# Performance work log

Measured on AMD Instinct MI355X. Metric: run time of the kernel, lower is better.

## Reference

```python
import jax, jax.numpy as jnp
import numpy as np

N, DIM, HEADS, E = 20000, 256, 4, 100000
C = DIM  # TransformerConv out_channels per head (concat=False averages heads)


def setup_inputs() -> dict:
    key = jax.random.key(0)
    ks = jax.random.split(key, 12)
    s = DIM ** -0.5
    w = lambda k, shape: jax.random.normal(k, shape, jnp.float32) * s
    z = lambda shape: jnp.zeros(shape, jnp.float32)
    return {
        "f_all": jax.random.normal(ks[0], (N, DIM), jnp.float32),
        "edge_index": jax.random.randint(ks[1], (2, E), 0, N),
        "W_gcn": w(ks[2], (DIM, DIM)), "b_gcn": z((DIM,)),
        "W_q": w(ks[3], (DIM, HEADS * C)), "b_q": z((HEADS * C,)),
        "W_k": w(ks[4], (DIM, HEADS * C)), "b_k": z((HEADS * C,)),
        "W_v": w(ks[5], (DIM, HEADS * C)), "b_v": z((HEADS * C,)),
        "W_skip": w(ks[6], (DIM, DIM)), "b_skip": z((DIM,)),
        "W_beta": w(ks[7], (3 * DIM, 1)),
        "W_cnn": w(ks[8], (DIM, DIM)), "b_cnn": z((DIM,)),
    }


def reference(f_all, edge_index, W_gcn, b_gcn, W_q, b_q, W_k, b_k, W_v, b_v,
              W_skip, b_skip, W_beta, W_cnn, b_cnn):
    src, dst = edge_index[0], edge_index[1]

    # --- GCNConv: add self loops, symmetric D^-1/2 (A+I) D^-1/2 normalization ---
    loop = jnp.arange(N)
    s2 = jnp.concatenate([src, loop])
    d2 = jnp.concatenate([dst, loop])
    deg = jax.ops.segment_sum(jnp.ones_like(d2, jnp.float32), d2, N)
    dinv = jnp.where(deg > 0, 1.0 / jnp.sqrt(deg), 0.0)
    norm = dinv[s2] * dinv[d2]                    # [E+N]
    h = f_all @ W_gcn                             # [N, DIM]
    x = jax.ops.segment_sum(h[s2] * norm[:, None], d2, N) + b_gcn
    x = jax.nn.relu(x)

    # --- TransformerConv(heads=H, concat=False, beta=True) ---
    q = (x @ W_q + b_q).reshape(N, HEADS, C)
    k = (x @ W_k + b_k).reshape(N, HEADS, C)
    v = (x @ W_v + b_v).reshape(N, HEADS, C)
    logits = jnp.einsum('ehc,ehc->eh', q[dst], k[src]) / np.float32(np.sqrt(C))
    m = jax.ops.segment_max(logits, dst, N)       # per-target max for stable softmax
    e = jnp.exp(logits - m[dst])
    denom = jax.ops.segment_sum(e, dst, N)
    alpha = e / jnp.maximum(denom[dst], 1e-16)    # [E, H]
    agg = jax.ops.segment_sum(v[src] * alpha[:, :, None], dst, N)  # [N, H, C]
    out = agg.mean(axis=1)                        # concat=False -> head average
    xr = x @ W_skip + b_skip                      # root/skip branch
    beta = jax.nn.sigmoid(jnp.concatenate([out, xr, out - xr], axis=-1) @ W_beta)
    tf = jax.nn.relu(beta * xr + (1.0 - beta) * out)  # [N, DIM]

    # --- Conv1d with kernel (dim,1) on [1,1,dim,N]: per-node linear, output [dim,N] ---
    conv = jnp.einsum('cd,nd->cn', W_cnn, tf) + b_cnn[:, None]  # [DIM, N]
    # torch does .view(1, n_mole, -1) on the [1,dim,1,N] conv output: raw reshape
    return conv.reshape(1, N, DIM)
```

## Files before the change

### kernel.cpp

```cpp
#include <hip/hip_runtime.h>
#include <math.h>

#define DIMC 256
#define NHEAD 4
#define CAP 64

typedef unsigned short bf16u;
typedef __attribute__((ext_vector_type(8))) short bf16x8;
typedef __attribute__((ext_vector_type(4))) float f32x4;

typedef __attribute__((address_space(1))) const unsigned char ga_u8;
typedef __attribute__((address_space(3))) unsigned char lds_u8;
__device__ __forceinline__ void gld_lds16(const void* g, void* l) {
    __builtin_amdgcn_global_load_lds((ga_u8*)g, (lds_u8*)l, 16, 0, 0);
}

__device__ __forceinline__ float bf2f(bf16u u) {
    union { float f; unsigned int i; } c; c.i = ((unsigned int)u) << 16; return c.f;
}
__device__ __forceinline__ bf16u f2bf(float f) {
    union { float f; unsigned int i; } c; c.f = f;
    unsigned int r = c.i + 0x7fffu + ((c.i >> 16) & 1u);
    return (bf16u)(r >> 16);
}
__device__ __forceinline__ void store_bf4(bf16u* p, float4 v) {
    ushort4 raw;
    raw.x = f2bf(v.x); raw.y = f2bf(v.y); raw.z = f2bf(v.z); raw.w = f2bf(v.w);
    *(ushort4*)p = raw;
}
__device__ __forceinline__ void load_bf8(const bf16u* p, float* o) {
    bf16x8 raw = *(const bf16x8*)p;
#pragma unroll
    for (int i = 0; i < 8; ++i) {
        union { float f; unsigned int u; } c;
        c.u = ((unsigned int)(unsigned short)raw[i]) << 16;
        o[i] = c.f;
    }
}
__device__ __forceinline__ void store_bf8(bf16u* p, const float* v) {
    bf16x8 raw;
#pragma unroll
    for (int i = 0; i < 8; ++i) raw[i] = (short)f2bf(v[i]);
    *(bf16x8*)p = raw;
}


__global__ void fill_kernel(const int* __restrict__ src, const int* __restrict__ dst,
                            int* __restrict__ cursor, int* __restrict__ srcs, int E) {
    int e = blockIdx.x * 256 + threadIdx.x;
    if (e < E) {
        int d = dst[e];
        int pos = atomicAdd(&cursor[d], 1);
        if (pos < CAP) srcs[d * CAP + pos] = src[e];
    }
}


__global__ __launch_bounds__(256) void prep_kernel(
    const float* __restrict__ f_all, int n4_f,
    const float* __restrict__ W_gcn, const float* __restrict__ W_q,
    const float* __restrict__ W_k, const float* __restrict__ W_v,
    const float* __restrict__ W_skip, const float* __restrict__ W_cnn,
    const float* __restrict__ b_q, const float* __restrict__ b_v,
    const float* __restrict__ b_skip,
    bf16u* __restrict__ xbuf, bf16u* __restrict__ WgcnT,
    bf16u* __restrict__ BTyp, bf16u* __restrict__ BT_vs,
    bf16u* __restrict__ Wcnn_b,
    float* __restrict__ ybias, float* __restrict__ bvm,
    int* __restrict__ cursor, int N) {
    __shared__ __align__(16) char sh[40960];
    int b = blockIdx.x, t = threadIdx.x;
    int nf = (n4_f + 255) >> 8;
    int nz = (N + 255) >> 8;

    if (b < 16) {
        bf16u (*As)[128][32] = (bf16u(*)[128][32])sh;
        bf16u (*Bs)[128][32] = (bf16u(*)[128][32])(sh + 16384);
        bf16u (*Cs)[128]     = (bf16u(*)[128])(sh + 32768);
        int rb = b >> 1, cb = b & 1;
        int h = rb >> 1;
        int j0 = (rb & 1) * 128;
        int t0 = h * 256;
        int w = t >> 6, lane = t & 63;
        int q = lane >> 4, r = lane & 15;
        int wm = (w & 1) * 64, wn = (w >> 1) * 64;
        int srow = t >> 2, scol = (t & 3) * 8;
        const float* ak0 = W_k + (size_t)(j0 + srow) * 1024 + t0 + scol;
        const float* ak1 = W_k + (size_t)(j0 + 64 + srow) * 1024 + t0 + scol;
        const float* bq0 = W_q + (size_t)(cb * 128 + srow) * 1024 + t0 + scol;
        const float* bq1 = W_q + (size_t)(cb * 128 + 64 + srow) * 1024 + t0 + scol;
        auto stage = [&](const float* gp, bf16u* lp) {
            float4 u = *(const float4*)gp, v = *(const float4*)(gp + 4);
            bf16x8 o;
            o[0] = (short)f2bf(u.x); o[1] = (short)f2bf(u.y);
            o[2] = (short)f2bf(u.z); o[3] = (short)f2bf(u.w);
            o[4] = (short)f2bf(v.x); o[5] = (short)f2bf(v.y);
            o[6] = (short)f2bf(v.z); o[7] = (short)f2bf(v.w);
            *(bf16x8*)lp = o;
        };
        f32x4 acc[4][4] = {};
        for (int g = 0; g < 4; ++g) {
            int k0 = g * 64;
            stage(ak0 + k0,      &As[0][srow][scol]);
            stage(ak1 + k0,      &As[0][64 + srow][scol]);
            stage(ak0 + k0 + 32, &As[1][srow][scol]);
            stage(ak1 + k0 + 32, &As[1][64 + srow][scol]);
            stage(bq0 + k0,      &Bs[0][srow][scol]);
            stage(bq1 + k0,      &Bs[0][64 + srow][scol]);
            stage(bq0 + k0 + 32, &Bs[1][srow][scol]);
            stage(bq1 + k0 + 32, &Bs[1][64 + srow][scol]);
            __syncthreads();
#pragma unroll
            for (int ks = 0; ks < 2; ++ks) {
                bf16x8 af[4], bfr[4];
#pragma unroll
                for (int i = 0; i < 4; ++i) af[i] = *(const bf16x8*)&As[ks][wm + i * 16 + r][q * 8];
#pragma unroll
                for (int j = 0; j < 4; ++j) bfr[j] = *(const bf16x8*)&Bs[ks][wn + j * 16 + r][q * 8];
#pragma unroll
                for (int i = 0; i < 4; ++i)
#pragma unroll
                    for (int j = 0; j < 4; ++j)
                        acc[i][j] = __builtin_amdgcn_mfma_f32_16x16x32_bf16(af[i], bfr[j], acc[i][j], 0, 0, 0);
            }
            __syncthreads();
        }
        int bm = rb * 128, bn = cb * 128;
        int rhalf = (w & 1) * 16;
        int colbase = (w >> 1) * 64;
#pragma unroll
        for (int i = 0; i < 4; ++i) {
#pragma unroll
            for (int j = 0; j < 4; ++j)
#pragma unroll
                for (int rg = 0; rg < 4; ++rg)
                    Cs[rhalf + q * 4 + rg][colbase + j * 16 + r] = f2bf(acc[i][j][rg] * 0.0625f);
            __syncthreads();
#pragma unroll
            for (int cpass = 0; cpass < 2; ++cpass) {
                int chunk = cpass * 256 + t;
                int sr = chunk >> 4;
                int c16 = chunk & 15;
                int grow = bm + (sr < 16 ? i * 16 + sr : 64 + i * 16 + (sr - 16));
                *(bf16x8*)&BTyp[(size_t)grow * 256 + bn + c16 * 8] = *(const bf16x8*)&Cs[sr][c16 * 8];
            }
            __syncthreads();
        }
        return;
    }
    b -= 16;
    if (b < nf) {
        int i = b * 256 + t;
        if (i < n4_f) {
            float4 vv = *(const float4*)(f_all + (size_t)i * 4);
            store_bf4(xbuf + (size_t)i * 4, vv);
        }
        return;
    }
    b -= nf;
    if (b < 64) {
        int i = b * 256 + t;
        float4 vv = *(const float4*)(W_cnn + (size_t)i * 4);
        store_bf4(Wcnn_b + (size_t)i * 4, vv);
        return;
    }
    b -= 64;
    if (b < 4) {
        int h = b, j = t;
        const float4* bq4 = (const float4*)(b_q + h * 256);
        const float4* wk4 = (const float4*)(W_k + (size_t)j * 1024 + h * 256);
        float acc = 0.f;
        for (int u = 0; u < 64; ++u) {
            float4 a = bq4[u], w = wk4[u];
            acc += a.x * w.x + a.y * w.y + a.z * w.z + a.w * w.w;
        }
        ybias[h * 256 + j] = acc * 0.0625f;
        return;
    }
    b -= 4;
    if (b < 1) {
        ybias[1024 + t] = b_skip[t];
        bvm[t] = 0.25f * (b_v[t] + b_v[256 + t] + b_v[512 + t] + b_v[768 + t]);
        return;
    }
    b -= 1;
    if (b < nz) {
        int i = b * 256 + t;
        if (i < N) cursor[i] = 0;
        return;
    }
    b -= nz;
    float (*T)[33] = (float(*)[33])sh;
    const float* src; bf16u* dst;
    int inld, inrow0, incol0, outld, outrow0, outcol0;
    if (b < 64) {
        int N0 = (b & 7) * 32, K0 = (b >> 3) * 32;
        src = W_gcn; inld = 256; inrow0 = K0; incol0 = N0;
        dst = WgcnT; outld = 256; outrow0 = N0; outcol0 = K0;
    } else if (b < 128) {
        int bb = b - 64; int N0 = (bb & 7) * 32, K0 = (bb >> 3) * 32;
        src = W_skip; inld = 256; inrow0 = K0; incol0 = N0;
        dst = BTyp;  outld = 256; outrow0 = 1024 + N0; outcol0 = K0;
    } else {
        int bb = b - 128; int jt = bb & 7, ct = (bb >> 3) & 7, hh = bb >> 6;
        src = W_v;  inld = 1024; inrow0 = ct * 32; incol0 = hh * 256 + jt * 32;
        dst = BT_vs; outld = 1024; outrow0 = jt * 32; outcol0 = hh * 256 + ct * 32;
    }
    int tx = t & 31, ty = t >> 5;
#pragma unroll
    for (int i = 0; i < 4; ++i)
        T[ty + 8 * i][tx] = src[(size_t)(inrow0 + ty + 8 * i) * inld + incol0 + tx];
    __syncthreads();
#pragma unroll
    for (int i = 0; i < 4; ++i)
        dst[(size_t)(outrow0 + ty + 8 * i) * outld + outcol0 + tx] = f2bf(T[tx][ty + 8 * i]);
}


template <bool ROWBIAS>
__global__ __launch_bounds__(256) void gemm_tile(const bf16u* __restrict__ A,
                                                 const bf16u* __restrict__ BT,
                                                 const float* __restrict__ bias,
                                                 void* __restrict__ Cout,
                                                 int M, int Nc, int ldc, int K) {
    __shared__ __align__(16) bf16u As[2][128][32];
    __shared__ __align__(16) bf16u Bs[2][128][32];
    int t = threadIdx.x;
    int w = t >> 6, lane = t & 63;
    int q = lane >> 4, r = lane & 15;
    int wm = (w & 1) * 64, wn = (w >> 1) * 64;
    int bm = blockIdx.y * 128, bn = blockIdx.x * 128;

    int srow = t >> 2, scol = (t & 3) * 8;
    int arow0 = bm + srow;      if (arow0 >= M)  arow0 = M - 1;
    int arow1 = bm + 64 + srow; if (arow1 >= M)  arow1 = M - 1;
    int brow0 = bn + srow;      if (brow0 >= Nc) brow0 = Nc - 1;
    int brow1 = bn + 64 + srow; if (brow1 >= Nc) brow1 = Nc - 1;
    const bf16u* a0 = A + (size_t)arow0 * K + scol;
    const bf16u* a1 = A + (size_t)arow1 * K + scol;
    const bf16u* b0 = BT + (size_t)brow0 * K + scol;
    const bf16u* b1 = BT + (size_t)brow1 * K + scol;

    char* As_base = (char*)&As[0][0][0] + w * 1024;
    char* Bs_base = (char*)&Bs[0][0][0] + w * 1024;

    f32x4 acc[4][4] = {};
    int ngroups = K >> 6;
    for (int g = 0; g < ngroups; ++g) {
        int k0 = g * 64;
        gld_lds16(a0 + k0, As_base);
        gld_lds16(a1 + k0, As_base + 4096);
        gld_lds16(b0 + k0, Bs_base);
        gld_lds16(b1 + k0, Bs_base + 4096);
        gld_lds16(a0 + k0 + 32, As_base + 8192);
        gld_lds16(a1 + k0 + 32, As_base + 8192 + 4096);
        gld_lds16(b0 + k0 + 32, Bs_base + 8192);
        gld_lds16(b1 + k0 + 32, Bs_base + 8192 + 4096);
        __syncthreads();
#pragma unroll
        for (int ks = 0; ks < 2; ++ks) {
            bf16x8 af[4], bfr[4];
#pragma unroll
            for (int i = 0; i < 4; ++i) af[i] = *(const bf16x8*)&As[ks][wm + i * 16 + r][q * 8];
#pragma unroll
            for (int j = 0; j < 4; ++j) bfr[j] = *(const bf16x8*)&Bs[ks][wn + j * 16 + r][q * 8];
#pragma unroll
            for (int i = 0; i < 4; ++i)
#pragma unroll
                for (int j = 0; j < 4; ++j)
                    acc[i][j] = __builtin_amdgcn_mfma_f32_16x16x32_bf16(af[i], bfr[j], acc[i][j], 0, 0, 0);
        }
        __syncthreads();
    }

    if (ROWBIAS) {
        float* C = (float*)Cout;
#pragma unroll
        for (int j = 0; j < 4; ++j) {
            int col = bn + wn + j * 16 + r;
            if (col >= Nc) continue;
#pragma unroll
            for (int i = 0; i < 4; ++i)
#pragma unroll
                for (int rg = 0; rg < 4; ++rg) {
                    int row = bm + wm + i * 16 + q * 4 + rg;
                    if (row < M)
                        __builtin_nontemporal_store(acc[i][j][rg] + bias[row],
                                                    &C[(size_t)row * ldc + col]);
                }
        }
    } else {
        __shared__ __align__(16) bf16u Cs[32][128];
        bf16u* C = (bf16u*)Cout;
        float cb4[4];
#pragma unroll
        for (int j = 0; j < 4; ++j) {
            int col = bn + wn + j * 16 + r;
            cb4[j] = bias ? bias[col] : 0.0f;
        }
        int rhalf = (w & 1) * 16;
        int colbase = (w >> 1) * 64;
        __syncthreads();
#pragma unroll
        for (int i = 0; i < 4; ++i) {
#pragma unroll
            for (int j = 0; j < 4; ++j)
#pragma unroll
                for (int rg = 0; rg < 4; ++rg)
                    Cs[rhalf + q * 4 + rg][colbase + j * 16 + r] = f2bf(acc[i][j][rg] + cb4[j]);
            __syncthreads();
#pragma unroll
            for (int cpass = 0; cpass < 2; ++cpass) {
                int chunk = cpass * 256 + t;
                int sr = chunk >> 4;
                int c16 = chunk & 15;
                int grow = bm + (sr < 16 ? i * 16 + sr : 64 + i * 16 + (sr - 16));
                if (grow < M)
                    __builtin_nontemporal_store(*(const bf16x8*)&Cs[sr][c16 * 8],
                                                (bf16x8*)&C[(size_t)grow * ldc + bn + c16 * 8]);
            }
            __syncthreads();
        }
    }
}


__global__ __launch_bounds__(256, 1) void zout_kernel(const bf16u* __restrict__ Z,
                                                      const bf16u* __restrict__ BT_vs,
                                                      const bf16u* __restrict__ Yp, int ldy,
                                                      const float* __restrict__ bvm,
                                                      const float* __restrict__ W_beta,
                                                      const int* __restrict__ cursor,
                                                      bf16u* __restrict__ tf, int M) {
    __shared__ __align__(16) char sh[53248];
    bf16u (*As)[128][32] = (bf16u(*)[128][32])sh;
    bf16u (*Bs)[256][32] = (bf16u(*)[256][32])(sh + 16384);
    bf16u (*Xr)[256]     = (bf16u(*)[256])sh;
    bf16u (*Cs)[256]     = (bf16u(*)[256])(sh + 16384);
    float* gateL = (float*)(sh + 49152);
    float* w13L  = (float*)(sh + 49664);
    float* w23L  = (float*)(sh + 50688);
    float* bvmL  = (float*)(sh + 51712);
    float* redL  = (float*)(sh + 52736);
    float* betL  = (float*)(sh + 52992);

    int t = threadIdx.x;
    int w = t >> 6, lane = t & 63;
    int q = lane >> 4, r = lane & 15;
    int wm = (w & 1) * 64, wmIdx = w & 1;
    int cg = w >> 1;
    int bm = blockIdx.x * 128;

    {
        float w1 = W_beta[t], w2 = W_beta[256 + t], w3 = W_beta[512 + t];
        w13L[t] = w1 + w3;
        w23L[t] = w2 - w3;
        bvmL[t] = bvm[t];
        if (t < 128) {
            int row = bm + t; if (row >= M) row = M - 1;
            gateL[t] = (cursor[row] > 0) ? 1.f : 0.f;
        }
    }

    int srow = t >> 2, scol = (t & 3) * 8;
    int arow0 = bm + srow;      if (arow0 >= M) arow0 = M - 1;
    int arow1 = bm + 64 + srow; if (arow1 >= M) arow1 = M - 1;
    const bf16u* a0 = Z + (size_t)arow0 * 1024 + scol;
    const bf16u* a1 = Z + (size_t)arow1 * 1024 + scol;
    const bf16u* bp[4];
#pragma unroll
    for (int h = 0; h < 4; ++h) bp[h] = BT_vs + (size_t)(h * 64 + srow) * 1024 + scol;

    char* As_base = (char*)sh + w * 1024;
    char* Bs_base = (char*)sh + 16384 + w * 1024;

    f32x4 acc[4][8] = {};
    for (int g = 0; g < 16; ++g) {
        int k0 = g * 64;
        gld_lds16(a0 + k0, As_base);
        gld_lds16(a1 + k0, As_base + 4096);
        gld_lds16(a0 + k0 + 32, As_base + 8192);
        gld_lds16(a1 + k0 + 32, As_base + 8192 + 4096);
#pragma unroll
        for (int h = 0; h < 4; ++h) {
            gld_lds16(bp[h] + k0, Bs_base + h * 4096);
            gld_lds16(bp[h] + k0 + 32, Bs_base + 16384 + h * 4096);
        }
        __syncthreads();
#pragma unroll
        for (int ks = 0; ks < 2; ++ks) {
            bf16x8 af[4], bfr[8];
#pragma unroll
            for (int i = 0; i < 4; ++i) af[i] = *(const bf16x8*)&As[ks][wm + i * 16 + r][q * 8];
#pragma unroll
            for (int j = 0; j < 8; ++j) {
                int brow = (j < 4 ? cg * 64 + j * 16 : 128 + cg * 64 + (j - 4) * 16) + r;
                bfr[j] = *(const bf16x8*)&Bs[ks][brow][q * 8];
            }
#pragma unroll
            for (int i = 0; i < 4; ++i)
#pragma unroll
                for (int j = 0; j < 8; ++j)
                    acc[i][j] = __builtin_amdgcn_mfma_f32_16x16x32_bf16(af[i], bfr[j], acc[i][j], 0, 0, 0);
        }
        __syncthreads();
    }

#pragma unroll
    for (int i = 0; i < 4; ++i) {
#pragma unroll
        for (int p = 0; p < 4; ++p) {
            int idx = p * 256 + t;
            int rowl = idx >> 5, ch = idx & 31;
            int grow = bm + (rowl < 16 ? i * 16 + rowl : 64 + i * 16 + (rowl - 16));
            if (grow >= M) grow = M - 1;
            gld_lds16(Yp + (size_t)grow * ldy + 1024 + ch * 8,
                      (char*)sh + p * 4096 + w * 1024);
        }
        __syncthreads();

        float contrib[4] = {0.f, 0.f, 0.f, 0.f};
#pragma unroll
        for (int j = 0; j < 8; ++j) {
            int col = (j < 4 ? cg * 64 + j * 16 : 128 + cg * 64 + (j - 4) * 16) + r;
            float w13c = w13L[col], w23c = w23L[col], bvc = bvmL[col];
#pragma unroll
            for (int rg = 0; rg < 4; ++rg) {
                int rowl32 = wmIdx * 16 + q * 4 + rg;
                float ov = acc[i][j][rg] + gateL[wm + i * 16 + q * 4 + rg] * bvc;
                float xr = bf2f(Xr[rowl32][col]);
                contrib[rg] += ov * w13c + xr * w23c;
            }
        }
#pragma unroll
        for (int rg = 0; rg < 4; ++rg)
#pragma unroll
            for (int msk = 1; msk <= 8; msk <<= 1)
                contrib[rg] += __shfl_xor(contrib[rg], msk, 64);
        if (r == 0) {
#pragma unroll
            for (int rg = 0; rg < 4; ++rg)
                redL[cg * 32 + wmIdx * 16 + q * 4 + rg] = contrib[rg];
        }
        __syncthreads();
        if (t < 32) betL[t] = 1.f / (1.f + __expf(-(redL[t] + redL[32 + t])));
        __syncthreads();

#pragma unroll
        for (int j = 0; j < 8; ++j) {
            int col = (j < 4 ? cg * 64 + j * 16 : 128 + cg * 64 + (j - 4) * 16) + r;
            float bvc = bvmL[col];
#pragma unroll
            for (int rg = 0; rg < 4; ++rg) {
                int rowl32 = wmIdx * 16 + q * 4 + rg;
                float bet = betL[rowl32];
                float ov = acc[i][j][rg] + gateL[wm + i * 16 + q * 4 + rg] * bvc;
                float xr = bf2f(Xr[rowl32][col]);
                Cs[rowl32][col] = f2bf(fmaxf(bet * xr + (1.f - bet) * ov, 0.f));
            }
        }
        __syncthreads();
#pragma unroll
        for (int p = 0; p < 4; ++p) {
            int idx = p * 256 + t;
            int sr = idx >> 5, c32 = idx & 31;
            int grow = bm + (sr < 16 ? i * 16 + sr : 64 + i * 16 + (sr - 16));
            if (grow < M)
                __builtin_nontemporal_store(*(const bf16x8*)&Cs[sr][c32 * 8],
                                            (bf16x8*)&tf[(size_t)grow * 256 + c32 * 8]);
        }
        __syncthreads();
    }
}


__global__ __launch_bounds__(256) void gcn_agg_kernel(const bf16u* __restrict__ h,
                                                      const int* __restrict__ cursor,
                                                      const int* __restrict__ srcs,
                                                      const float* __restrict__ b_gcn,
                                                      bf16u* __restrict__ x, int N) {
    int n = blockIdx.x * 8 + (threadIdx.x >> 5);
    if (n >= N) return;
    int lane = threadIdx.x & 31;
    int cb = lane * 8;
    int cnt = cursor[n]; if (cnt > CAP) cnt = CAP;
    float dn = rsqrtf((float)(cnt + 1));
    float hn[8];
    load_bf8(h + (size_t)n * DIMC + cb, hn);
    int base = n * CAP;
    float acc[8] = {};
    int i = 0;
    for (; i + 4 <= cnt; i += 4) {
        int4 s4 = *(const int4*)(srcs + base + i);
        float d0 = rsqrtf((float)(cursor[s4.x] + 1));
        float d1 = rsqrtf((float)(cursor[s4.y] + 1));
        float d2 = rsqrtf((float)(cursor[s4.z] + 1));
        float d3 = rsqrtf((float)(cursor[s4.w] + 1));
        float h0[8], h1[8], h2[8], h3[8];
        load_bf8(h + (size_t)s4.x * DIMC + cb, h0);
        load_bf8(h + (size_t)s4.y * DIMC + cb, h1);
        load_bf8(h + (size_t)s4.z * DIMC + cb, h2);
        load_bf8(h + (size_t)s4.w * DIMC + cb, h3);
#pragma unroll
        for (int j = 0; j < 8; ++j)
            acc[j] += h0[j] * d0 + h1[j] * d1 + h2[j] * d2 + h3[j] * d3;
    }
    for (; i < cnt; ++i) {
        int s = srcs[base + i];
        float ds = rsqrtf((float)(cursor[s] + 1));
        float hv[8];
        load_bf8(h + (size_t)s * DIMC + cb, hv);
#pragma unroll
        for (int j = 0; j < 8; ++j) acc[j] += hv[j] * ds;
    }
    float4 bg0 = *(const float4*)(b_gcn + cb);
    float4 bg1 = *(const float4*)(b_gcn + cb + 4);
    float bg[8] = {bg0.x, bg0.y, bg0.z, bg0.w, bg1.x, bg1.y, bg1.z, bg1.w};
    float dnn = dn * dn;
    float o[8];
#pragma unroll
    for (int j = 0; j < 8; ++j) o[j] = fmaxf(dn * acc[j] + hn[j] * dnn + bg[j], 0.f);
    store_bf8(x + (size_t)n * DIMC + cb, o);
}


__global__ __launch_bounds__(256) void attn_kernel(const bf16u* __restrict__ Y, int ldy,
                                                   const bf16u* __restrict__ x,
                                                   const int* __restrict__ cursor,
                                                   const int* __restrict__ srcs,
                                                   bf16u* __restrict__ Z, int N) {
    __shared__ __align__(16) bf16u xs[4][2][256];
    int wv = threadIdx.x >> 6;
    int n = blockIdx.x * 4 + wv;
    if (n >= N) return;
    int lane = threadIdx.x & 63;
    int hq = lane >> 4;
    int r = lane & 15;

    float yv[16];
    const bf16u* yrow = Y + (size_t)n * ldy + hq * DIMC + r * 16;
    load_bf8(yrow, yv);
    load_bf8(yrow + 8, yv + 8);

    int cnt = cursor[n]; if (cnt > CAP) cnt = CAP;
    int base = n * CAP;
    float m = -INFINITY, denom = 0.f;
    float acc[16];
#pragma unroll
    for (int j = 0; j < 16; ++j) acc[j] = 0.f;

    int rl = lane >> 5;
    int rc = (lane & 31) * 8;
    bf16u* myslot = &xs[wv][rl][rc];

    int iters = (cnt + 1) >> 1;
    int i0 = 0, i1 = 0;
    if (cnt > 1) {
        int2 ss = *(const int2*)(srcs + base);
        i0 = ss.x; i1 = ss.y;
    } else if (cnt == 1) {
        i0 = srcs[base]; i1 = i0;
    }
    bf16x8 raw;
    if (iters > 0)
        raw = *(const bf16x8*)(x + (size_t)(rl ? i1 : i0) * DIMC + rc);

    for (int it = 0; it < iters; ++it) {
        *(bf16x8*)myslot = raw;
        int e2 = (it + 1) * 2;
        int nv2 = cnt - e2;
        if (nv2 > 1) {
            int2 ss = *(const int2*)(srcs + base + e2);
            i0 = ss.x; i1 = ss.y;
        } else if (nv2 == 1) {
            i0 = srcs[base + e2]; i1 = i0;
        }
        if (nv2 > 0)
            raw = *(const bf16x8*)(x + (size_t)(rl ? i1 : i0) * DIMC + rc);
        asm volatile("s_waitcnt lgkmcnt(0)" ::: "memory");
        float x0[16], x1[16];
        load_bf8(&xs[wv][0][r * 16], x0);
        load_bf8(&xs[wv][0][r * 16 + 8], x0 + 8);
        load_bf8(&xs[wv][1][r * 16], x1);
        load_bf8(&xs[wv][1][r * 16 + 8], x1 + 8);
        float d0 = 0.f, d1 = 0.f;
#pragma unroll
        for (int j = 0; j < 16; ++j) { d0 += yv[j] * x0[j]; d1 += yv[j] * x1[j]; }
#pragma unroll
        for (int msk = 1; msk <= 8; msk <<= 1) {
            d0 += __shfl_xor(d0, msk, 64);
            d1 += __shfl_xor(d1, msk, 64);
        }
        if ((cnt & 1) && it == iters - 1) d1 = -INFINITY;
        float pm = fmaxf(d0, d1);
        if (pm > m + 8.f) {
            float so = __expf(m - pm);
            denom *= so;
#pragma unroll
            for (int j = 0; j < 16; ++j) acc[j] *= so;
            m = pm;
        }
        float p0 = __expf(d0 - m);
        float p1 = __expf(d1 - m);
        denom += p0 + p1;
#pragma unroll
        for (int j = 0; j < 16; ++j) acc[j] += p0 * x0[j] + p1 * x1[j];
        asm volatile("" ::: "memory");
    }

    float inv = 0.25f / fmaxf(denom, 1e-16f);
    float o[16];
#pragma unroll
    for (int j = 0; j < 16; ++j) o[j] = acc[j] * inv;
    bf16u* zrow = Z + (size_t)n * 1024 + hq * DIMC + r * 16;
    store_bf8(zrow, o);
    store_bf8(zrow + 8, o + 8);
}


static inline size_t align_up(size_t x) { return (x + 255) & ~(size_t)255; }

extern "C" void kernel_launch(void* const* d_in, const int* in_sizes, int n_in,
                              void* d_out, int out_size, void* d_ws, size_t ws_size,
                              hipStream_t stream) {
    const float* f_all  = (const float*)d_in[0];
    const int*   eidx   = (const int*)d_in[1];
    const float* W_gcn  = (const float*)d_in[2];
    const float* b_gcn  = (const float*)d_in[3];
    const float* W_q    = (const float*)d_in[4];
    const float* b_q    = (const float*)d_in[5];
    const float* W_k    = (const float*)d_in[6];
    const float* W_v    = (const float*)d_in[8];
    const float* b_v    = (const float*)d_in[9];
    const float* W_skip = (const float*)d_in[10];
    const float* b_skip = (const float*)d_in[11];
    const float* W_beta = (const float*)d_in[12];
    const float* W_cnn  = (const float*)d_in[13];
    const float* b_cnn  = (const float*)d_in[14];

    const int N = in_sizes[0] / DIMC;
    const int E = in_sizes[1] / 2;
    const int* src = eidx;
    const int* dst = eidx + E;

    char* p = (char*)d_ws;
    auto alloc = [&](size_t bytes) { char* r = p; p += align_up(bytes); return r; };
    int*   cursor = (int*)alloc((size_t)N * 4);
    int*   srcs   = (int*)alloc((size_t)N * CAP * 4);
    bf16u* WgcnT  = (bf16u*)alloc(256 * 256 * 2);
    bf16u* BTyp   = (bf16u*)alloc((size_t)1280 * 256 * 2);
    bf16u* BT_vs  = (bf16u*)alloc((size_t)256 * 1024 * 2);
    bf16u* Wcnn_b = (bf16u*)alloc(256 * 256 * 2);
    float* ybias  = (float*)alloc(1280 * 4);
    float* bvm    = (float*)alloc(256 * 4);
    bf16u* xbuf   = (bf16u*)alloc((size_t)N * DIMC * 2);
    bf16u* h      = (bf16u*)alloc((size_t)N * DIMC * 2);
    bf16u* Yp     = (bf16u*)alloc((size_t)N * 1280 * 2);
    bf16u* Z      = (bf16u*)alloc((size_t)N * 1024 * 2);

    int n4_f = N * DIMC / 4;
    int nf = (n4_f + 255) >> 8;
    int nz = (N + 255) >> 8;
    prep_kernel<<<16 + nf + 64 + 4 + 1 + nz + 384, 256, 0, stream>>>(
        f_all, n4_f, W_gcn, W_q, W_k, W_v, W_skip, W_cnn,
        b_q, b_v, b_skip, xbuf, WgcnT, BTyp, BT_vs, Wcnn_b,
        ybias, bvm, cursor, N);

    fill_kernel<<<(E + 255) / 256, 256, 0, stream>>>(src, dst, cursor, srcs, E);

    int mby = (N + 127) / 128;
    gemm_tile<false><<<dim3(2, mby), 256, 0, stream>>>(xbuf, WgcnT, nullptr, h, N, 256, 256, 256);
    gcn_agg_kernel<<<(N + 7) / 8, 256, 0, stream>>>(h, cursor, srcs, b_gcn, xbuf, N);
    gemm_tile<false><<<dim3(10, mby), 256, 0, stream>>>(xbuf, BTyp, ybias, Yp, N, 1280, 1280, 256);
    attn_kernel<<<(N + 3) / 4, 256, 0, stream>>>(Yp, 1280, xbuf, cursor, srcs, Z, N);
    zout_kernel<<<mby, 256, 0, stream>>>(Z, BT_vs, Yp, 1280, bvm, W_beta, cursor, h, N);
    gemm_tile<true><<<dim3((N + 127) / 128, 2), 256, 0, stream>>>(
        Wcnn_b, h, b_cnn, (float*)d_out, 256, N, N, 256);
}
```

Baseline: 258.1 us.

## Precompute beta gate in attention kernel via folded W_v·W_beta, split zout over columns

The beta gate logit is computed algebraically in the attention kernel by folding W_v with (W_beta1+W_beta3) into a per-head vector u plus a bias constant, so the gate no longer needs the full 256-column Z@Wv output. This lets the output GEMM be split into two 128-column tiles per row block (doubling the grid and cutting per-block registers and LDS). The cost is extra per-node dot products and Yp reads in attention, plus a few prep blocks to compute u and c0. The gate is now formed from bf16 Z values rather than fp32 accumulators, which may change rounding slightly.

```diff
diff --git a/kernel.cpp b/kernel.cpp
--- a/kernel.cpp
+++ b/kernel.cpp
@@ -62,11 +62,12 @@
     const float* __restrict__ W_k, const float* __restrict__ W_v,
     const float* __restrict__ W_skip, const float* __restrict__ W_cnn,
     const float* __restrict__ b_q, const float* __restrict__ b_v,
-    const float* __restrict__ b_skip,
+    const float* __restrict__ b_skip, const float* __restrict__ W_beta,
     bf16u* __restrict__ xbuf, bf16u* __restrict__ WgcnT,
     bf16u* __restrict__ BTyp, bf16u* __restrict__ BT_vs,
     bf16u* __restrict__ Wcnn_b,
     float* __restrict__ ybias, float* __restrict__ bvm,
+    float* __restrict__ ubuf, float* __restrict__ c0p,
     int* __restrict__ cursor, int N) {
     __shared__ __align__(16) char sh[40960];
     int b = blockIdx.x, t = threadIdx.x;
@@ -184,6 +185,35 @@
         return;
     }
     b -= 1;
+    if (b < 4) {
+        int h = b, d = t;
+        const float4* wb1 = (const float4*)W_beta;
+        const float4* wb3 = (const float4*)(W_beta + 512);
+        const float4* wv4 = (const float4*)(W_v + (size_t)d * 1024 + h * 256);
+        float acc = 0.f;
+        for (int uu = 0; uu < 64; ++uu) {
+            float4 a = wb1[uu], c = wb3[uu], w = wv4[uu];
+            acc += (a.x + c.x) * w.x + (a.y + c.y) * w.y
+                 + (a.z + c.z) * w.z + (a.w + c.w) * w.w;
+        }
+        ubuf[h * 256 + d] = acc;
+        return;
+    }
+    b -= 4;
+    if (b < 1) {
+        float* red = (float*)sh;
+        float w13 = W_beta[t] + W_beta[512 + t];
+        float bv = 0.25f * (b_v[t] + b_v[256 + t] + b_v[512 + t] + b_v[768 + t]);
+        red[t] = w13 * bv;
+        __syncthreads();
+        for (int s = 128; s > 0; s >>= 1) {
+            if (t < s) red[t] += red[t + s];
+            __syncthreads();
+        }
+        if (t == 0) c0p[0] = red[0];
+        return;
+    }
+    b -= 1;
     if (b < nz) {
         int i = b * 256 + t;
         if (i < N) cursor[i] = 0;
@@ -325,149 +355,108 @@
 }
 
 
-__global__ __launch_bounds__(256, 1) void zout_kernel(const bf16u* __restrict__ Z,
-                                                      const bf16u* __restrict__ BT_vs,
-                                                      const bf16u* __restrict__ Yp, int ldy,
-                                                      const float* __restrict__ bvm,
-                                                      const float* __restrict__ W_beta,
-                                                      const int* __restrict__ cursor,
-                                                      bf16u* __restrict__ tf, int M) {
-    __shared__ __align__(16) char sh[53248];
-    bf16u (*As)[128][32] = (bf16u(*)[128][32])sh;
-    bf16u (*Bs)[256][32] = (bf16u(*)[256][32])(sh + 16384);
-    bf16u (*Xr)[256]     = (bf16u(*)[256])sh;
-    bf16u (*Cs)[256]     = (bf16u(*)[256])(sh + 16384);
-    float* gateL = (float*)(sh + 49152);
-    float* w13L  = (float*)(sh + 49664);
-    float* w23L  = (float*)(sh + 50688);
-    float* bvmL  = (float*)(sh + 51712);
-    float* redL  = (float*)(sh + 52736);
-    float* betL  = (float*)(sh + 52992);
-
+__global__ __launch_bounds__(256) void ztf_kernel(const bf16u* __restrict__ Z,
+                                                  const bf16u* __restrict__ BT_vs,
+                                                  const bf16u* __restrict__ Yp, int ldy,
+                                                  const float* __restrict__ bvm,
+                                                  const float* __restrict__ betaArr,
+                                                  const int* __restrict__ cursor,
+                                                  bf16u* __restrict__ tf, int M) {
+    __shared__ __align__(16) bf16u As[2][128][32];
+    __shared__ __align__(16) bf16u Bs[2][128][32];
+    __shared__ __align__(16) bf16u Cs[32][128];
+    const int K = 1024;
     int t = threadIdx.x;
     int w = t >> 6, lane = t & 63;
     int q = lane >> 4, r = lane & 15;
-    int wm = (w & 1) * 64, wmIdx = w & 1;
-    int cg = w >> 1;
-    int bm = blockIdx.x * 128;
-
-    {
-        float w1 = W_beta[t], w2 = W_beta[256 + t], w3 = W_beta[512 + t];
-        w13L[t] = w1 + w3;
-        w23L[t] = w2 - w3;
-        bvmL[t] = bvm[t];
-        if (t < 128) {
-            int row = bm + t; if (row >= M) row = M - 1;
-            gateL[t] = (cursor[row] > 0) ? 1.f : 0.f;
-        }
-    }
+    int wm = (w & 1) * 64, wn = (w >> 1) * 64;
+    int bm = blockIdx.y * 128, bn = blockIdx.x * 128;
 
     int srow = t >> 2, scol = (t & 3) * 8;
     int arow0 = bm + srow;      if (arow0 >= M) arow0 = M - 1;
     int arow1 = bm + 64 + srow; if (arow1 >= M) arow1 = M - 1;
-    const bf16u* a0 = Z + (size_t)arow0 * 1024 + scol;
-    const bf16u* a1 = Z + (size_t)arow1 * 1024 + scol;
-    const bf16u* bp[4];
-#pragma unroll
-    for (int h = 0; h < 4; ++h) bp[h] = BT_vs + (size_t)(h * 64 + srow) * 1024 + scol;
-
-    char* As_base = (char*)sh + w * 1024;
-    char* Bs_base = (char*)sh + 16384 + w * 1024;
-
-    f32x4 acc[4][8] = {};
+    const bf16u* a0 = Z + (size_t)arow0 * K + scol;
+    const bf16u* a1 = Z + (size_t)arow1 * K + scol;
+    const bf16u* b0 = BT_vs + (size_t)(bn + srow) * K + scol;
+    const bf16u* b1 = BT_vs + (size_t)(bn + 64 + srow) * K + scol;
+
+    char* As_base = (char*)&As[0][0][0] + w * 1024;
+    char* Bs_base = (char*)&Bs[0][0][0] + w * 1024;
+
+    f32x4 acc[4][4] = {};
     for (int g = 0; g < 16; ++g) {
         int k0 = g * 64;
         gld_lds16(a0 + k0, As_base);
         gld_lds16(a1 + k0, As_base + 4096);
+        gld_lds16(b0 + k0, Bs_base);
+        gld_lds16(b1 + k0, Bs_base + 4096);
         gld_lds16(a0 + k0 + 32, As_base + 8192);
         gld_lds16(a1 + k0 + 32, As_base + 8192 + 4096);
-#pragma unroll
-        for (int h = 0; h < 4; ++h) {
-            gld_lds16(bp[h] + k0, Bs_base + h * 4096);
-            gld_lds16(bp[h] + k0 + 32, Bs_base + 16384 + h * 4096);
-        }
+        gld_lds16(b0 + k0 + 32, Bs_base + 8192);
+        gld_lds16(b1 + k0 + 32, Bs_base + 8192 + 4096);
         __syncthreads();
 #pragma unroll
         for (int ks = 0; ks < 2; ++ks) {
-            bf16x8 af[4], bfr[8];
+            bf16x8 af[4], bfr[4];
 #pragma unroll
             for (int i = 0; i < 4; ++i) af[i] = *(const bf16x8*)&As[ks][wm + i * 16 + r][q * 8];
 #pragma unroll
-            for (int j = 0; j < 8; ++j) {
-                int brow = (j < 4 ? cg * 64 + j * 16 : 128 + cg * 64 + (j - 4) * 16) + r;
-                bfr[j] = *(const bf16x8*)&Bs[ks][brow][q * 8];
+            for (int j = 0; j < 4; ++j) bfr[j] = *(const bf16x8*)&Bs[ks][wn + j * 16 + r][q * 8];
+#pragma unroll
+            for (int i = 0; i < 4; ++i)
+#pragma unroll
+                for (int j = 0; j < 4; ++j)
+                    acc[i][j] = __builtin_amdgcn_mfma_f32_16x16x32_bf16(af[i], bfr[j], acc[i][j], 0, 0, 0);
+        }
+        __syncthreads();
+    }
+
+    int rhalf = (w & 1) * 16;
+    int colbase = (w >> 1) * 64;
+    char* Xr_base = (char*)&As[0][0][0];
+    bf16u (*Xr)[128] = (bf16u(*)[128])Xr_base;
+#pragma unroll
+    for (int i = 0; i < 4; ++i) {
+#pragma unroll
+        for (int p = 0; p < 2; ++p) {
+            int idx = p * 256 + t;
+            int sr = idx >> 4, c16 = idx & 15;
+            int grow = bm + (sr < 16 ? i * 16 + sr : 64 + i * 16 + (sr - 16));
+            if (grow >= M) grow = M - 1;
+            gld_lds16(Yp + (size_t)grow * ldy + 1024 + bn + c16 * 8,
+                      Xr_base + p * 4096 + w * 1024);
+        }
+        __syncthreads();
+        float bet[4], gate[4];
+#pragma unroll
+        for (int rg = 0; rg < 4; ++rg) {
+            int growR = bm + wm + i * 16 + q * 4 + rg;
+            if (growR >= M) growR = M - 1;
+            bet[rg] = betaArr[growR];
+            gate[rg] = (cursor[growR] > 0) ? 1.f : 0.f;
+        }
+#pragma unroll
+        for (int j = 0; j < 4; ++j) {
+            int col = colbase + j * 16 + r;
+            float bv = bvm[bn + col];
+#pragma unroll
+            for (int rg = 0; rg < 4; ++rg) {
+                float ov = acc[i][j][rg] + gate[rg] * bv;
+                float xr = bf2f(Xr[rhalf + q * 4 + rg][col]);
+                Cs[rhalf + q * 4 + rg][col] =
+                    f2bf(fmaxf(bet[rg] * xr + (1.f - bet[rg]) * ov, 0.f));
             }
-#pragma unroll
-            for (int i = 0; i < 4; ++i)
-#pragma unroll
-                for (int j = 0; j < 8; ++j)
-                    acc[i][j] = __builtin_amdgcn_mfma_f32_16x16x32_bf16(af[i], bfr[j], acc[i][j], 0, 0, 0);
-        }
-        __syncthreads();
-    }
-
-#pragma unroll
-    for (int i = 0; i < 4; ++i) {
-#pragma unroll
-        for (int p = 0; p < 4; ++p) {
-            int idx = p * 256 + t;
-            int rowl = idx >> 5, ch = idx & 31;
-            int grow = bm + (rowl < 16 ? i * 16 + rowl : 64 + i * 16 + (rowl - 16));
-            if (grow >= M) grow = M - 1;
-            gld_lds16(Yp + (size_t)grow * ldy + 1024 + ch * 8,
-                      (char*)sh + p * 4096 + w * 1024);
-        }
-        __syncthreads();
-
-        float contrib[4] = {0.f, 0.f, 0.f, 0.f};
-#pragma unroll
-        for (int j = 0; j < 8; ++j) {
-            int col = (j < 4 ? cg * 64 + j * 16 : 128 + cg * 64 + (j - 4) * 16) + r;
-            float w13c = w13L[col], w23c = w23L[col], bvc = bvmL[col];
-#pragma unroll
-            for (int rg = 0; rg < 4; ++rg) {
-                int rowl32 = wmIdx * 16 + q * 4 + rg;
-                float ov = acc[i][j][rg] + gateL[wm + i * 16 + q * 4 + rg] * bvc;
-                float xr = bf2f(Xr[rowl32][col]);
-                contrib[rg] += ov * w13c + xr * w23c;
-            }
-        }
-#pragma unroll
-        for (int rg = 0; rg < 4; ++rg)
-#pragma unroll
-            for (int msk = 1; msk <= 8; msk <<= 1)
-                contrib[rg] += __shfl_xor(contrib[rg], msk, 64);
-        if (r == 0) {
-#pragma unroll
-            for (int rg = 0; rg < 4; ++rg)
-                redL[cg * 32 + wmIdx * 16 + q * 4 + rg] = contrib[rg];
-        }
-        __syncthreads();
-        if (t < 32) betL[t] = 1.f / (1.f + __expf(-(redL[t] + redL[32 + t])));
-        __syncthreads();
-
-#pragma unroll
-        for (int j = 0; j < 8; ++j) {
-            int col = (j < 4 ? cg * 64 + j * 16 : 128 + cg * 64 + (j - 4) * 16) + r;
-            float bvc = bvmL[col];
-#pragma unroll
-            for (int rg = 0; rg < 4; ++rg) {
-                int rowl32 = wmIdx * 16 + q * 4 + rg;
-                float bet = betL[rowl32];
-                float ov = acc[i][j][rg] + gateL[wm + i * 16 + q * 4 + rg] * bvc;
-                float xr = bf2f(Xr[rowl32][col]);
-                Cs[rowl32][col] = f2bf(fmaxf(bet * xr + (1.f - bet) * ov, 0.f));
-            }
-        }
-        __syncthreads();
-#pragma unroll
-        for (int p = 0; p < 4; ++p) {
-            int idx = p * 256 + t;
-            int sr = idx >> 5, c32 = idx & 31;
+        }
+        __syncthreads();
+#pragma unroll
+        for (int cpass = 0; cpass < 2; ++cpass) {
+            int chunk = cpass * 256 + t;
+            int sr = chunk >> 4;
+            int c16 = chunk & 15;
             int grow = bm + (sr < 16 ? i * 16 + sr : 64 + i * 16 + (sr - 16));
             if (grow < M)
-                __builtin_nontemporal_store(*(const bf16x8*)&Cs[sr][c32 * 8],
-                                            (bf16x8*)&tf[(size_t)grow * 256 + c32 * 8]);
+                __builtin_nontemporal_store(*(const bf16x8*)&Cs[sr][c16 * 8],
+                                            (bf16x8*)&tf[(size_t)grow * 256 + bn + c16 * 8]);
         }
         __syncthreads();
     }
@@ -528,7 +517,11 @@
                                                    const bf16u* __restrict__ x,
                                                    const int* __restrict__ cursor,
                                                    const int* __restrict__ srcs,
-                                                   bf16u* __restrict__ Z, int N) {
+                                                   const float* __restrict__ u,
+                                                   const float* __restrict__ c0p,
+                                                   const float* __restrict__ W_beta,
+                                                   bf16u* __restrict__ Z,
+                                                   float* __restrict__ betaArr, int N) {
     __shared__ __align__(16) bf16u xs[4][2][256];
     int wv = threadIdx.x >> 6;
     int n = blockIdx.x * 4 + wv;
@@ -615,6 +608,27 @@
     bf16u* zrow = Z + (size_t)n * 1024 + hq * DIMC + r * 16;
     store_bf8(zrow, o);
     store_bf8(zrow + 8, o + 8);
+
+    float bp = 0.f;
+#pragma unroll
+    for (int j = 0; j < 16; ++j) bp += o[j] * u[hq * 256 + r * 16 + j];
+    float xv2[16];
+    load_bf8(Y + (size_t)n * ldy + 1024 + r * 16, xv2);
+    load_bf8(Y + (size_t)n * ldy + 1024 + r * 16 + 8, xv2 + 8);
+    float xp = 0.f;
+#pragma unroll
+    for (int j = 0; j < 16; ++j)
+        xp += xv2[j] * (W_beta[256 + r * 16 + j] - W_beta[512 + r * 16 + j]);
+#pragma unroll
+    for (int msk = 1; msk <= 8; msk <<= 1) {
+        bp += __shfl_xor(bp, msk, 64);
+        xp += __shfl_xor(xp, msk, 64);
+    }
+    bp += __shfl_xor(bp, 16, 64);
+    bp += __shfl_xor(bp, 32, 64);
+    float gate = (cnt > 0) ? 1.f : 0.f;
+    float contrib = bp + xp + gate * c0p[0];
+    if (lane == 0) betaArr[n] = 1.f / (1.f + __expf(-contrib));
 }
 
 
@@ -645,26 +659,29 @@
 
     char* p = (char*)d_ws;
     auto alloc = [&](size_t bytes) { char* r = p; p += align_up(bytes); return r; };
-    int*   cursor = (int*)alloc((size_t)N * 4);
-    int*   srcs   = (int*)alloc((size_t)N * CAP * 4);
-    bf16u* WgcnT  = (bf16u*)alloc(256 * 256 * 2);
-    bf16u* BTyp   = (bf16u*)alloc((size_t)1280 * 256 * 2);
-    bf16u* BT_vs  = (bf16u*)alloc((size_t)256 * 1024 * 2);
-    bf16u* Wcnn_b = (bf16u*)alloc(256 * 256 * 2);
-    float* ybias  = (float*)alloc(1280 * 4);
-    float* bvm    = (float*)alloc(256 * 4);
-    bf16u* xbuf   = (bf16u*)alloc((size_t)N * DIMC * 2);
-    bf16u* h      = (bf16u*)alloc((size_t)N * DIMC * 2);
-    bf16u* Yp     = (bf16u*)alloc((size_t)N * 1280 * 2);
-    bf16u* Z      = (bf16u*)alloc((size_t)N * 1024 * 2);
+    int*   cursor  = (int*)alloc((size_t)N * 4);
+    int*   srcs    = (int*)alloc((size_t)N * CAP * 4);
+    bf16u* WgcnT   = (bf16u*)alloc(256 * 256 * 2);
+    bf16u* BTyp    = (bf16u*)alloc((size_t)1280 * 256 * 2);
+    bf16u* BT_vs   = (bf16u*)alloc((size_t)256 * 1024 * 2);
+    bf16u* Wcnn_b  = (bf16u*)alloc(256 * 256 * 2);
+    float* ybias   = (float*)alloc(1280 * 4);
+    float* bvm     = (float*)alloc(256 * 4);
+    float* ubuf    = (float*)alloc(1024 * 4);
+    float* c0p     = (float*)alloc(256);
+    float* betaArr = (float*)alloc((size_t)N * 4);
+    bf16u* xbuf    = (bf16u*)alloc((size_t)N * DIMC * 2);
+    bf16u* h       = (bf16u*)alloc((size_t)N * DIMC * 2);
+    bf16u* Yp      = (bf16u*)alloc((size_t)N * 1280 * 2);
+    bf16u* Z       = (bf16u*)alloc((size_t)N * 1024 * 2);
 
     int n4_f = N * DIMC / 4;
     int nf = (n4_f + 255) >> 8;
     int nz = (N + 255) >> 8;
-    prep_kernel<<<16 + nf + 64 + 4 + 1 + nz + 384, 256, 0, stream>>>(
+    prep_kernel<<<16 + nf + 64 + 4 + 1 + 4 + 1 + nz + 384, 256, 0, stream>>>(
         f_all, n4_f, W_gcn, W_q, W_k, W_v, W_skip, W_cnn,
-        b_q, b_v, b_skip, xbuf, WgcnT, BTyp, BT_vs, Wcnn_b,
-        ybias, bvm, cursor, N);
+        b_q, b_v, b_skip, W_beta, xbuf, WgcnT, BTyp, BT_vs, Wcnn_b,
+        ybias, bvm, ubuf, c0p, cursor, N);
 
     fill_kernel<<<(E + 255) / 256, 256, 0, stream>>>(src, dst, cursor, srcs, E);
 
@@ -672,8 +689,10 @@
     gemm_tile<false><<<dim3(2, mby), 256, 0, stream>>>(xbuf, WgcnT, nullptr, h, N, 256, 256, 256);
     gcn_agg_kernel<<<(N + 7) / 8, 256, 0, stream>>>(h, cursor, srcs, b_gcn, xbuf, N);
     gemm_tile<false><<<dim3(10, mby), 256, 0, stream>>>(xbuf, BTyp, ybias, Yp, N, 1280, 1280, 256);
-    attn_kernel<<<(N + 3) / 4, 256, 0, stream>>>(Yp, 1280, xbuf, cursor, srcs, Z, N);
-    zout_kernel<<<mby, 256, 0, stream>>>(Z, BT_vs, Yp, 1280, bvm, W_beta, cursor, h, N);
+    attn_kernel<<<(N + 3) / 4, 256, 0, stream>>>(Yp, 1280, xbuf, cursor, srcs,
+                                                 ubuf, c0p, W_beta, Z, betaArr, N);
+    ztf_kernel<<<dim3(2, mby), 256, 0, stream>>>(Z, BT_vs, Yp, 1280, bvm, betaArr,
+                                                 cursor, h, N);
     gemm_tile<true><<<dim3((N + 127) / 128, 2), 256, 0, stream>>>(
         Wcnn_b, h, b_cnn, (float*)d_out, 256, N, N, 256);
 }
```

Measured after the change: 257.1 us. No clear change (-0.4%).
